# Kernel optimization log

Hardware: AMD Instinct MI355X
Metric: run time of the kernel (lower is better)

Reference implementation:

```python
import jax, jax.numpy as jnp
import numpy as np

C_SINGLE = 768
C_PAIR = 128
NUM_HEADS = 16
D_HEAD = C_SINGLE // NUM_HEADS
LC = 1024


def setup_inputs() -> dict:
    key = jax.random.key(0)
    ks = jax.random.split(key, 16)
    s = jax.random.normal(ks[0], (LC, C_SINGLE), dtype=jnp.float32)
    z = jax.random.normal(ks[1], (LC, LC, C_PAIR), dtype=jnp.float32)
    pd_mask = jax.random.randint(ks[2], (LC, LC), 0, 2) > 0
    pd_mask = pd_mask | jnp.eye(LC, dtype=bool)  # ensure every row has a valid key
    dist_bias_h = jax.random.normal(ks[3], (LC, LC, NUM_HEADS), dtype=jnp.float32)
    prior_bias = jax.random.normal(ks[4], (LC, LC), dtype=jnp.float32)
    def lin_w(k):
        return jax.random.normal(k, (C_SINGLE, C_SINGLE), dtype=jnp.float32) * 0.02
    def lin_b(k):
        return jax.random.normal(k, (C_SINGLE,), dtype=jnp.float32) * 0.02
    return {
        "s": s, "z": z, "pd_mask": pd_mask,
        "dist_bias_h": dist_bias_h, "prior_bias": prior_bias,
        "Wq": lin_w(ks[5]), "bq": lin_b(ks[6]),
        "Wk": lin_w(ks[7]), "bk": lin_b(ks[8]),
        "Wv": lin_w(ks[9]), "bv": lin_b(ks[10]),
        "Wz": jax.random.normal(ks[11], (C_PAIR, NUM_HEADS), dtype=jnp.float32) * 0.02,
        "Wo": lin_w(ks[12]), "bo": lin_b(ks[13]),
        "Wg": lin_w(ks[14]), "bg": lin_b(ks[15]),
    }


def reference(s, z, pd_mask, dist_bias_h, prior_bias,
              Wq, bq, Wk, bk, Wv, bv, Wz, Wo, bo, Wg, bg):
    Lc = s.shape[0]
    H, d = NUM_HEADS, D_HEAD
    # projections, split heads -> [H, Lc, d]
    qh = (s @ Wq + bq).reshape(Lc, H, d).transpose(1, 0, 2)
    kh = (s @ Wk + bk).reshape(Lc, H, d).transpose(1, 0, 2)
    vh = (s @ Wv + bv).reshape(Lc, H, d).transpose(1, 0, 2)
    scale = 1.0 / (d ** 0.5)
    # fp32 logits (module forces fp32 for attention block)
    logits = jnp.einsum('hid,hjd->hij',
                        qh.astype(jnp.float32), kh.astype(jnp.float32)) * scale
    # pair bias: [Lc,Lc,c_pair] @ [c_pair,H] -> [H,Lc,Lc]
    logits = logits + jnp.einsum('ijc,ch->hij', z.astype(jnp.float32), Wz)
    logits = logits + dist_bias_h.astype(jnp.float32).transpose(2, 0, 1)
    logits = logits + prior_bias.astype(jnp.float32)[None]
    neg_inf = jnp.finfo(jnp.float32).min
    logits = jnp.where(pd_mask[None], logits, neg_inf)
    attn = jax.nn.softmax(logits, axis=-1)
    # dropout is identity in eval mode
    attn_c = attn.astype(s.dtype)
    ctx = jnp.einsum('hij,hjd->hid', attn_c, vh)
    ctx = ctx.transpose(1, 0, 2).reshape(Lc, H * d)
    gate = jax.nn.sigmoid(s @ Wg + bg)
    y = gate * (ctx @ Wo + bo)
    return y, attn_c
```

## Files before the change

kernel.cpp:

```cpp
#include <hip/hip_runtime.h>
#include <hip/hip_bf16.h>
#include <float.h>

#define LC 1024
#define CS 768
#define NH 16
#define DH 48
#define CP 128

typedef __attribute__((ext_vector_type(8))) short short8;
typedef __attribute__((ext_vector_type(4))) float f32x4;
typedef __attribute__((ext_vector_type(4))) unsigned short ushort4v;

__device__ inline unsigned short f2b(float f){
    unsigned u = __builtin_bit_cast(unsigned, f);
    unsigned r = 0x7FFFu + ((u >> 16) & 1u);
    return (unsigned short)((u + r) >> 16);
}

__global__ void k_convert(const float* __restrict__ src, unsigned short* __restrict__ dst, int n){
    int i = (blockIdx.x * blockDim.x + threadIdx.x) * 4;
    if (i < n){
        float4 v = *reinterpret_cast<const float4*>(src + i);
        ushort4v o;
        o[0] = f2b(v.x); o[1] = f2b(v.y); o[2] = f2b(v.z); o[3] = f2b(v.w);
        *reinterpret_cast<ushort4v*>(dst + i) = o;
    }
}

struct P5 { const float* s[5]; unsigned short* d[5]; };

__global__ void k_transpose_w5(P5 p){
    __shared__ float t[32][33];
    int m = blockIdx.z;
    const float* W = p.s[m];
    unsigned short* O = p.d[m];
    int i0 = blockIdx.x * 32, o0 = blockIdx.y * 32;
    int tx = threadIdx.x & 31, ty = threadIdx.x >> 5;
    for (int r = 0; r < 32; r += 8)
        t[ty + r][tx] = W[(long)(i0 + ty + r) * CS + o0 + tx];
    __syncthreads();
    for (int r = 0; r < 32; r += 8)
        O[(long)(o0 + ty + r) * CS + i0 + tx] = f2b(t[tx][ty + r]);
}

__global__ void k_transpose_v(const unsigned short* __restrict__ v, unsigned short* __restrict__ vt){
    __shared__ unsigned short t[32][33];
    int j0 = blockIdx.x * 32, c0 = blockIdx.y * 32;
    int tx = threadIdx.x & 31, ty = threadIdx.x >> 5;
    for (int r = 0; r < 32; r += 8)
        t[ty + r][tx] = v[(long)(j0 + ty + r) * CS + c0 + tx];
    __syncthreads();
    for (int r = 0; r < 32; r += 8)
        vt[(long)(c0 + ty + r) * LC + j0 + tx] = t[tx][ty + r];
}

__global__ __launch_bounds__(256) void k_gemm(
    const unsigned short* __restrict__ A,
    const unsigned short* __restrict__ B,
    const float* __restrict__ bias,
    void* __restrict__ out,
    const float* __restrict__ gate,
    int mode)
{
    __shared__ unsigned short As[64][40];
    __shared__ unsigned short Bs[64][40];
    int m0 = blockIdx.x * 64, n0 = blockIdx.y * 64;
    int t = threadIdx.x, lane = t & 63, w = t >> 6;
    int l15 = lane & 15, l4 = lane >> 4;
    f32x4 zero4 = {0.f, 0.f, 0.f, 0.f};
    f32x4 acc[4] = {zero4, zero4, zero4, zero4};

    for (int kk = 0; kk < CS; kk += 32){
        int row = t >> 2, c = (t & 3) * 8;
        *reinterpret_cast<short8*>(&As[row][c]) =
            *reinterpret_cast<const short8*>(&A[(long)(m0 + row) * CS + kk + c]);
        *reinterpret_cast<short8*>(&Bs[row][c]) =
            *reinterpret_cast<const short8*>(&B[(long)(n0 + row) * CS + kk + c]);
        __syncthreads();
        short8 af = *reinterpret_cast<const short8*>(&As[w * 16 + l15][l4 * 8]);
        for (int nt = 0; nt < 4; nt++){
            short8 bf = *reinterpret_cast<const short8*>(&Bs[nt * 16 + l15][l4 * 8]);
            acc[nt] = __builtin_amdgcn_mfma_f32_16x16x32_bf16(af, bf, acc[nt], 0, 0, 0);
        }
        __syncthreads();
    }
    for (int nt = 0; nt < 4; nt++){
        int col = n0 + nt * 16 + l15;
        float bv = bias[col];
        for (int r = 0; r < 4; r++){
            int rowi = m0 + w * 16 + l4 * 4 + r;
            float v = acc[nt][r] + bv;
            if (mode <= 2){
                ((unsigned short*)out)[(long)rowi * CS + col] = f2b(v);
            } else if (mode == 3){
                ((float*)out)[(long)rowi * CS + col] = 1.0f / (1.0f + expf(-v));
            } else {
                ((float*)out)[(long)rowi * CS + col] = gate[(long)rowi * CS + col] * v;
            }
        }
    }
}

__global__ __launch_bounds__(512) void k_logits(
    const float* __restrict__ z,
    const float* __restrict__ Wz,
    const unsigned short* __restrict__ qb,
    const unsigned short* __restrict__ kb,
    const float* __restrict__ dist,
    const float* __restrict__ prior,
    const int* __restrict__ mask,
    float* __restrict__ attn,
    float* __restrict__ stats)
{
    __shared__ float Ls[16][16][17];
    __shared__ float dist_s[16][16][17];
    __shared__ float prior_s[16][16];
    __shared__ int   mask_s[16][16];

    int I0 = blockIdx.x * 16;
    int chunk = blockIdx.y;
    int t = threadIdx.x, lane = t & 63, w = t >> 6;
    int l15 = lane & 15, l4 = lane >> 4;
    const float scale = 0.14433756729740643f;

    short8 wzf[4];
    for (int ck = 0; ck < 4; ck++){
        short8 f;
        for (int b = 0; b < 8; b++){
            int c = ck * 32 + l4 * 8 + b;
            f[b] = (short)f2b(Wz[c * 16 + l15]);
        }
        wzf[ck] = f;
    }
    short8 qf0[2], qf1[2];
    for (int rep = 0; rep < 2; rep++){
        int h = w * 2 + rep;
        const unsigned short* qrow = qb + (long)(I0 + l15) * CS + h * 48;
        qf0[rep] = *reinterpret_cast<const short8*>(qrow + l4 * 8);
        short8 zz; for (int b = 0; b < 8; b++) zz[b] = 0;
        qf1[rep] = zz;
        if (l4 < 2) qf1[rep] = *reinterpret_cast<const short8*>(qrow + 32 + l4 * 8);
    }

    float mreg[8], sreg[8];
    for (int p = 0; p < 8; p++){ mreg[p] = -FLT_MAX; sreg[p] = 0.f; }

    for (int jt = 0; jt < 8; jt++){
        int j0 = chunk * 128 + jt * 16;

        for (int rep = 0; rep < 2; rep++){
            int i = w * 2 + rep;
            f32x4 acc = {0.f, 0.f, 0.f, 0.f};
            const float* zrow = z + ((long)(I0 + i) * LC + (j0 + l15)) * CP;
            for (int ck = 0; ck < 4; ck++){
                float4 z0 = *reinterpret_cast<const float4*>(zrow + ck * 32 + l4 * 8);
                float4 z1 = *reinterpret_cast<const float4*>(zrow + ck * 32 + l4 * 8 + 4);
                short8 zf;
                zf[0] = f2b(z0.x); zf[1] = f2b(z0.y); zf[2] = f2b(z0.z); zf[3] = f2b(z0.w);
                zf[4] = f2b(z1.x); zf[5] = f2b(z1.y); zf[6] = f2b(z1.z); zf[7] = f2b(z1.w);
                acc = __builtin_amdgcn_mfma_f32_16x16x32_bf16(zf, wzf[ck], acc, 0, 0, 0);
            }
            for (int r = 0; r < 4; r++) Ls[i][l4 * 4 + r][l15] = acc[r];
        }
        {
            int s = t * 8;
            int di = s >> 8, rem = s & 255;
            const float* src = dist + (((long)(I0 + di) * LC + j0) * NH) + rem;
            float4 d0 = *reinterpret_cast<const float4*>(src);
            float4 d1 = *reinterpret_cast<const float4*>(src + 4);
            float dv[8] = {d0.x, d0.y, d0.z, d0.w, d1.x, d1.y, d1.z, d1.w};
            for (int b = 0; b < 8; b++){
                int jj = (rem + b) >> 4, hh = (rem + b) & 15;
                dist_s[di][jj][hh] = dv[b];
            }
            if (t < 256){
                int ii = t >> 4, jj = t & 15;
                prior_s[ii][jj] = prior[(long)(I0 + ii) * LC + j0 + jj];
                mask_s[ii][jj]  = mask [(long)(I0 + ii) * LC + j0 + jj];
            }
        }
        __syncthreads();

        for (int rep = 0; rep < 2; rep++){
            int h = w * 2 + rep;
            const unsigned short* krow = kb + (long)(j0 + l15) * CS + h * 48;
            short8 kf0 = *reinterpret_cast<const short8*>(krow + l4 * 8);
            short8 kf1; for (int b = 0; b < 8; b++) kf1[b] = 0;
            if (l4 < 2) kf1 = *reinterpret_cast<const short8*>(krow + 32 + l4 * 8);
            f32x4 acc = {0.f, 0.f, 0.f, 0.f};
            acc = __builtin_amdgcn_mfma_f32_16x16x32_bf16(qf0[rep], kf0, acc, 0, 0, 0);
            acc = __builtin_amdgcn_mfma_f32_16x16x32_bf16(qf1[rep], kf1, acc, 0, 0, 0);
            for (int r = 0; r < 4; r++)
                Ls[l4 * 4 + r][l15][h] += acc[r] * scale;
        }
        __syncthreads();

        int qw = t >> 4, jl = t & 15;
        for (int p = 0; p < 8; p++){
            int task = p * 32 + qw;
            int ti = task >> 4, th = task & 15;
            float lg = Ls[ti][jl][th] + dist_s[ti][jl][th] + prior_s[ti][jl];
            bool mk = (mask_s[ti][jl] != 0);
            lg = mk ? lg : -FLT_MAX;
            attn[(long)th * LC * LC + (long)(I0 + ti) * LC + j0 + jl] = lg;
            float mt = lg;
            for (int mo = 1; mo < 16; mo <<= 1) mt = fmaxf(mt, __shfl_xor(mt, mo));
            float e = mk ? expf(lg - mt) : 0.f;
            float st = e;
            for (int mo = 1; mo < 16; mo <<= 1) st += __shfl_xor(st, mo);
            if (mt > mreg[p]){
                sreg[p] = sreg[p] * expf(mreg[p] - mt) + st;
                mreg[p] = mt;
            } else {
                sreg[p] += st * expf(mt - mreg[p]);
            }
        }
        __syncthreads();
    }
    if ((t & 15) == 0){
        int qw = t >> 4;
        for (int p = 0; p < 8; p++){
            int task = p * 32 + qw;
            int ti = task >> 4, th = task & 15;
            long off = (((long)th * LC + (I0 + ti)) * 8 + chunk) * 2;
            stats[off]     = mreg[p];
            stats[off + 1] = sreg[p];
        }
    }
}

__global__ __launch_bounds__(256) void k_ctx(
    float* __restrict__ attn,
    const unsigned short* __restrict__ vt,
    const float* __restrict__ stats,
    unsigned short* __restrict__ ctx)
{
    int h = blockIdx.x, ib = blockIdx.y;
    int t = threadIdx.x, lane = t & 63, w = t >> 6;
    int l15 = lane & 15, l4 = lane >> 4;
    int i = ib * 64 + w * 16 + l15;

    const float* sp = stats + ((long)h * LC + i) * 16;
    float M = -FLT_MAX;
    for (int c = 0; c < 8; c++) M = fmaxf(M, sp[c * 2]);
    float S = 0.f;
    for (int c = 0; c < 8; c++) S += sp[c * 2 + 1] * expf(sp[c * 2] - M);
    float invS = 1.0f / S;

    f32x4 zero4 = {0.f, 0.f, 0.f, 0.f};
    f32x4 acc[3] = {zero4, zero4, zero4};
    float* arow = attn + (long)h * LC * LC + (long)i * LC;

    for (int jk = 0; jk < LC; jk += 32){
        float4 a0 = *reinterpret_cast<const float4*>(arow + jk + l4 * 8);
        float4 a1 = *reinterpret_cast<const float4*>(arow + jk + l4 * 8 + 4);
        float p[8] = {a0.x, a0.y, a0.z, a0.w, a1.x, a1.y, a1.z, a1.w};
        short8 pf;
        for (int b = 0; b < 8; b++){
            float e = expf(p[b] - M) * invS;
            p[b] = e;
            pf[b] = (short)f2b(e);
        }
        float4 o0 = {p[0], p[1], p[2], p[3]}, o1 = {p[4], p[5], p[6], p[7]};
        *reinterpret_cast<float4*>(arow + jk + l4 * 8) = o0;
        *reinterpret_cast<float4*>(arow + jk + l4 * 8 + 4) = o1;
        for (int dt = 0; dt < 3; dt++){
            const unsigned short* vrow = vt + (long)(h * 48 + dt * 16 + l15) * LC + jk + l4 * 8;
            short8 bf = *reinterpret_cast<const short8*>(vrow);
            acc[dt] = __builtin_amdgcn_mfma_f32_16x16x32_bf16(pf, bf, acc[dt], 0, 0, 0);
        }
    }
    for (int dt = 0; dt < 3; dt++)
        for (int r = 0; r < 4; r++){
            int rowi = ib * 64 + w * 16 + l4 * 4 + r;
            ctx[(long)rowi * CS + h * 48 + dt * 16 + l15] = f2b(acc[dt][r]);
        }
}

extern "C" void kernel_launch(void* const* d_in, const int* in_sizes, int n_in,
                              void* d_out, int out_size, void* d_ws, size_t ws_size,
                              hipStream_t stream)
{
    const float* s     = (const float*)d_in[0];
    const float* z     = (const float*)d_in[1];
    const int*   mask  = (const int*)  d_in[2];
    const float* dist  = (const float*)d_in[3];
    const float* prior = (const float*)d_in[4];
    const float* Wq = (const float*)d_in[5];  const float* bq = (const float*)d_in[6];
    const float* Wk = (const float*)d_in[7];  const float* bk = (const float*)d_in[8];
    const float* Wv = (const float*)d_in[9];  const float* bv = (const float*)d_in[10];
    const float* Wz = (const float*)d_in[11];
    const float* Wo = (const float*)d_in[12]; const float* bo = (const float*)d_in[13];
    const float* Wg = (const float*)d_in[14]; const float* bg = (const float*)d_in[15];

    char* ws = (char*)d_ws;
    const size_t SZ_BF = (size_t)LC * CS * 2;
    const size_t SZ_WT = (size_t)CS * CS * 2;
    unsigned short* sb   = (unsigned short*)(ws);
    unsigned short* wqt  = (unsigned short*)(ws + SZ_BF);
    unsigned short* wkt  = (unsigned short*)(ws + SZ_BF + SZ_WT);
    unsigned short* wvt  = (unsigned short*)(ws + SZ_BF + 2 * SZ_WT);
    unsigned short* wgt  = (unsigned short*)(ws + SZ_BF + 3 * SZ_WT);
    unsigned short* wot  = (unsigned short*)(ws + SZ_BF + 4 * SZ_WT);
    unsigned short* qb   = (unsigned short*)(ws + SZ_BF + 5 * SZ_WT);
    unsigned short* kb   = (unsigned short*)(ws + 2 * SZ_BF + 5 * SZ_WT);
    unsigned short* vb   = (unsigned short*)(ws + 3 * SZ_BF + 5 * SZ_WT);
    unsigned short* vt   = (unsigned short*)(ws + 4 * SZ_BF + 5 * SZ_WT);
    float*          gate = (float*)        (ws + 5 * SZ_BF + 5 * SZ_WT);
    unsigned short* ctxb = (unsigned short*)(ws + 5 * SZ_BF + 5 * SZ_WT + (size_t)LC * CS * 4);
    float*          stats= (float*)        (ws + 6 * SZ_BF + 5 * SZ_WT + (size_t)LC * CS * 4);

    float* y    = (float*)d_out;
    float* attn = (float*)d_out + (size_t)LC * CS;

    k_convert<<<768, 256, 0, stream>>>(s, sb, LC * CS);
    P5 p;
    p.s[0] = Wq; p.s[1] = Wk; p.s[2] = Wv; p.s[3] = Wg; p.s[4] = Wo;
    p.d[0] = wqt; p.d[1] = wkt; p.d[2] = wvt; p.d[3] = wgt; p.d[4] = wot;
    k_transpose_w5<<<dim3(24, 24, 5), 256, 0, stream>>>(p);

    k_gemm<<<dim3(16, 12), 256, 0, stream>>>(sb, wqt, bq, qb, nullptr, 0);
    k_gemm<<<dim3(16, 12), 256, 0, stream>>>(sb, wkt, bk, kb, nullptr, 1);
    k_gemm<<<dim3(16, 12), 256, 0, stream>>>(sb, wvt, bv, vb, nullptr, 2);
    k_gemm<<<dim3(16, 12), 256, 0, stream>>>(sb, wgt, bg, gate, nullptr, 3);
    k_transpose_v<<<dim3(32, 24), 256, 0, stream>>>(vb, vt);

    k_logits<<<dim3(64, 8), 512, 0, stream>>>(z, Wz, qb, kb, dist, prior, mask, attn, stats);
    k_ctx<<<dim3(16, 16), 256, 0, stream>>>(attn, vt, stats, ctxb);
    k_gemm<<<dim3(16, 12), 256, 0, stream>>>(ctxb, wot, bo, y, gate, 4);
}
```

Measured before the change: 1.004 ms.

## Fuse QKVG GEMMs, prefetch z/dist in logits, split ctx over key halves

Merges the four projection GEMMs into one launch over concatenated transposed weights. In the logits kernel, it register-prefetches the next tile's z, dist, prior and mask, drops one barrier by writing QK scores to a separate shared buffer, and uses fast exp with a branchless online-softmax update. The ctx kernel splits the key range across two waves and reduces them through shared memory, doubling the grid for more parallelism. The trade-offs are higher register pressure and a launch_bounds occupancy hint in the logits kernel, plus slightly less precise exponentials.

```diff
diff --git a/kernel.cpp b/kernel.cpp
--- a/kernel.cpp
+++ b/kernel.cpp
@@ -55,13 +55,61 @@
         vt[(long)(c0 + ty + r) * LC + j0 + tx] = t[tx][ty + r];
 }
 
-__global__ __launch_bounds__(256) void k_gemm(
+__global__ __launch_bounds__(256) void k_gemm_qkvg(
+    const unsigned short* __restrict__ A,
+    const unsigned short* __restrict__ B,
+    const float* __restrict__ bq, const float* __restrict__ bk,
+    const float* __restrict__ bv, const float* __restrict__ bg,
+    unsigned short* __restrict__ oq, unsigned short* __restrict__ ok,
+    unsigned short* __restrict__ ov, float* __restrict__ og)
+{
+    __shared__ unsigned short As[64][40];
+    __shared__ unsigned short Bs[64][40];
+    int m0 = blockIdx.x * 64, n0 = blockIdx.y * 64;
+    int seg = blockIdx.y / 12;
+    int ncol0 = n0 - seg * CS;
+    int t = threadIdx.x, lane = t & 63, w = t >> 6;
+    int l15 = lane & 15, l4 = lane >> 4;
+    f32x4 zero4 = {0.f, 0.f, 0.f, 0.f};
+    f32x4 acc[4] = {zero4, zero4, zero4, zero4};
+
+    for (int kk = 0; kk < CS; kk += 32){
+        int row = t >> 2, c = (t & 3) * 8;
+        *reinterpret_cast<short8*>(&As[row][c]) =
+            *reinterpret_cast<const short8*>(&A[(long)(m0 + row) * CS + kk + c]);
+        *reinterpret_cast<short8*>(&Bs[row][c]) =
+            *reinterpret_cast<const short8*>(&B[(long)(n0 + row) * CS + kk + c]);
+        __syncthreads();
+        short8 af = *reinterpret_cast<const short8*>(&As[w * 16 + l15][l4 * 8]);
+        for (int nt = 0; nt < 4; nt++){
+            short8 bf = *reinterpret_cast<const short8*>(&Bs[nt * 16 + l15][l4 * 8]);
+            acc[nt] = __builtin_amdgcn_mfma_f32_16x16x32_bf16(af, bf, acc[nt], 0, 0, 0);
+        }
+        __syncthreads();
+    }
+    const float* bias = (seg == 0) ? bq : (seg == 1) ? bk : (seg == 2) ? bv : bg;
+    unsigned short* obf = (seg == 0) ? oq : (seg == 1) ? ok : ov;
+    for (int nt = 0; nt < 4; nt++){
+        int col = ncol0 + nt * 16 + l15;
+        float bvv = bias[col];
+        for (int r = 0; r < 4; r++){
+            int rowi = m0 + w * 16 + l4 * 4 + r;
+            float v = acc[nt][r] + bvv;
+            if (seg < 3){
+                obf[(long)rowi * CS + col] = f2b(v);
+            } else {
+                og[(long)rowi * CS + col] = 1.0f / (1.0f + __expf(-v));
+            }
+        }
+    }
+}
+
+__global__ __launch_bounds__(256) void k_gemm_out(
     const unsigned short* __restrict__ A,
     const unsigned short* __restrict__ B,
     const float* __restrict__ bias,
-    void* __restrict__ out,
     const float* __restrict__ gate,
-    int mode)
+    float* __restrict__ out)
 {
     __shared__ unsigned short As[64][40];
     __shared__ unsigned short Bs[64][40];
@@ -87,22 +135,15 @@
     }
     for (int nt = 0; nt < 4; nt++){
         int col = n0 + nt * 16 + l15;
-        float bv = bias[col];
+        float bvv = bias[col];
         for (int r = 0; r < 4; r++){
             int rowi = m0 + w * 16 + l4 * 4 + r;
-            float v = acc[nt][r] + bv;
-            if (mode <= 2){
-                ((unsigned short*)out)[(long)rowi * CS + col] = f2b(v);
-            } else if (mode == 3){
-                ((float*)out)[(long)rowi * CS + col] = 1.0f / (1.0f + expf(-v));
-            } else {
-                ((float*)out)[(long)rowi * CS + col] = gate[(long)rowi * CS + col] * v;
-            }
-        }
-    }
-}
-
-__global__ __launch_bounds__(512) void k_logits(
+            out[(long)rowi * CS + col] = gate[(long)rowi * CS + col] * (acc[nt][r] + bvv);
+        }
+    }
+}
+
+__global__ __launch_bounds__(512, 4) void k_logits(
     const float* __restrict__ z,
     const float* __restrict__ Wz,
     const unsigned short* __restrict__ qb,
@@ -113,7 +154,8 @@
     float* __restrict__ attn,
     float* __restrict__ stats)
 {
-    __shared__ float Ls[16][16][17];
+    __shared__ float Ls [16][16][17];
+    __shared__ float Ls2[16][16][17];
     __shared__ float dist_s[16][16][17];
     __shared__ float prior_s[16][16];
     __shared__ int   mask_s[16][16];
@@ -146,42 +188,86 @@
     float mreg[8], sreg[8];
     for (int p = 0; p < 8; p++){ mreg[p] = -FLT_MAX; sreg[p] = 0.f; }
 
+    float4 pf[8];
+    float4 dd0, dd1;
+    float pp = 0.f; int mm = 0;
+    int sofs = t * 8, di = sofs >> 8, rem = sofs & 255;
+    int pr_i = t >> 4, pr_j = t & 15;
+
+    int row0 = I0 + w * 2;
+
     for (int jt = 0; jt < 8; jt++){
         int j0 = chunk * 128 + jt * 16;
 
-        for (int rep = 0; rep < 2; rep++){
-            int i = w * 2 + rep;
+        if (jt == 0){
+            const float* zr = z + ((long)row0 * LC + (j0 + l15)) * CP + l4 * 8;
+            pf[0] = *(const float4*)(zr);      pf[1] = *(const float4*)(zr + 4);
+            pf[2] = *(const float4*)(zr + 32); pf[3] = *(const float4*)(zr + 36);
+            pf[4] = *(const float4*)(zr + 64); pf[5] = *(const float4*)(zr + 68);
+            pf[6] = *(const float4*)(zr + 96); pf[7] = *(const float4*)(zr + 100);
+            const float* dsrc = dist + (((long)(I0 + di) * LC + j0) * NH) + rem;
+            dd0 = *(const float4*)dsrc; dd1 = *(const float4*)(dsrc + 4);
+            if (t < 256){
+                pp = prior[(long)(I0 + pr_i) * LC + j0 + pr_j];
+                mm = mask [(long)(I0 + pr_i) * LC + j0 + pr_j];
+            }
+        }
+
+        {
+            float dv[8] = {dd0.x, dd0.y, dd0.z, dd0.w, dd1.x, dd1.y, dd1.z, dd1.w};
+            #pragma unroll
+            for (int b = 0; b < 8; b++){
+                int jj = (rem + b) >> 4, hh = (rem + b) & 15;
+                dist_s[di][jj][hh] = dv[b];
+            }
+            if (t < 256){ prior_s[pr_i][pr_j] = pp; mask_s[pr_i][pr_j] = mm; }
+        }
+
+        {
             f32x4 acc = {0.f, 0.f, 0.f, 0.f};
-            const float* zrow = z + ((long)(I0 + i) * LC + (j0 + l15)) * CP;
+            #pragma unroll
             for (int ck = 0; ck < 4; ck++){
-                float4 z0 = *reinterpret_cast<const float4*>(zrow + ck * 32 + l4 * 8);
-                float4 z1 = *reinterpret_cast<const float4*>(zrow + ck * 32 + l4 * 8 + 4);
+                float4 z0 = pf[ck * 2], z1 = pf[ck * 2 + 1];
                 short8 zf;
                 zf[0] = f2b(z0.x); zf[1] = f2b(z0.y); zf[2] = f2b(z0.z); zf[3] = f2b(z0.w);
                 zf[4] = f2b(z1.x); zf[5] = f2b(z1.y); zf[6] = f2b(z1.z); zf[7] = f2b(z1.w);
                 acc = __builtin_amdgcn_mfma_f32_16x16x32_bf16(zf, wzf[ck], acc, 0, 0, 0);
             }
-            for (int r = 0; r < 4; r++) Ls[i][l4 * 4 + r][l15] = acc[r];
+            #pragma unroll
+            for (int r = 0; r < 4; r++) Ls[w * 2][l4 * 4 + r][l15] = acc[r];
         }
         {
-            int s = t * 8;
-            int di = s >> 8, rem = s & 255;
-            const float* src = dist + (((long)(I0 + di) * LC + j0) * NH) + rem;
-            float4 d0 = *reinterpret_cast<const float4*>(src);
-            float4 d1 = *reinterpret_cast<const float4*>(src + 4);
-            float dv[8] = {d0.x, d0.y, d0.z, d0.w, d1.x, d1.y, d1.z, d1.w};
-            for (int b = 0; b < 8; b++){
-                int jj = (rem + b) >> 4, hh = (rem + b) & 15;
-                dist_s[di][jj][hh] = dv[b];
-            }
+            const float* zr = z + ((long)(row0 + 1) * LC + (j0 + l15)) * CP + l4 * 8;
+            f32x4 acc = {0.f, 0.f, 0.f, 0.f};
+            #pragma unroll
+            for (int ck = 0; ck < 4; ck++){
+                float4 z0 = *(const float4*)(zr + ck * 32);
+                float4 z1 = *(const float4*)(zr + ck * 32 + 4);
+                short8 zf;
+                zf[0] = f2b(z0.x); zf[1] = f2b(z0.y); zf[2] = f2b(z0.z); zf[3] = f2b(z0.w);
+                zf[4] = f2b(z1.x); zf[5] = f2b(z1.y); zf[6] = f2b(z1.z); zf[7] = f2b(z1.w);
+                acc = __builtin_amdgcn_mfma_f32_16x16x32_bf16(zf, wzf[ck], acc, 0, 0, 0);
+            }
+            #pragma unroll
+            for (int r = 0; r < 4; r++) Ls[w * 2 + 1][l4 * 4 + r][l15] = acc[r];
+        }
+
+        if (jt < 7){
+            int j0n = j0 + 16;
+            const float* zr = z + ((long)row0 * LC + (j0n + l15)) * CP + l4 * 8;
+            pf[0] = *(const float4*)(zr);      pf[1] = *(const float4*)(zr + 4);
+            pf[2] = *(const float4*)(zr + 32); pf[3] = *(const float4*)(zr + 36);
+            pf[4] = *(const float4*)(zr + 64); pf[5] = *(const float4*)(zr + 68);
+            pf[6] = *(const float4*)(zr + 96); pf[7] = *(const float4*)(zr + 100);
+            const float* dsrc = dist + (((long)(I0 + di) * LC + j0n) * NH) + rem;
+            dd0 = *(const float4*)dsrc; dd1 = *(const float4*)(dsrc + 4);
             if (t < 256){
-                int ii = t >> 4, jj = t & 15;
-                prior_s[ii][jj] = prior[(long)(I0 + ii) * LC + j0 + jj];
-                mask_s[ii][jj]  = mask [(long)(I0 + ii) * LC + j0 + jj];
-            }
-        }
-        __syncthreads();
-
+                pp = prior[(long)(I0 + pr_i) * LC + j0n + pr_j];
+                mm = mask [(long)(I0 + pr_i) * LC + j0n + pr_j];
+            }
+        }
+
+        #pragma unroll
         for (int rep = 0; rep < 2; rep++){
             int h = w * 2 + rep;
             const unsigned short* krow = kb + (long)(j0 + l15) * CS + h * 48;
@@ -191,35 +277,35 @@
             f32x4 acc = {0.f, 0.f, 0.f, 0.f};
             acc = __builtin_amdgcn_mfma_f32_16x16x32_bf16(qf0[rep], kf0, acc, 0, 0, 0);
             acc = __builtin_amdgcn_mfma_f32_16x16x32_bf16(qf1[rep], kf1, acc, 0, 0, 0);
+            #pragma unroll
             for (int r = 0; r < 4; r++)
-                Ls[l4 * 4 + r][l15][h] += acc[r] * scale;
+                Ls2[l4 * 4 + r][l15][h] = acc[r] * scale;
         }
         __syncthreads();
 
         int qw = t >> 4, jl = t & 15;
+        #pragma unroll
         for (int p = 0; p < 8; p++){
             int task = p * 32 + qw;
             int ti = task >> 4, th = task & 15;
-            float lg = Ls[ti][jl][th] + dist_s[ti][jl][th] + prior_s[ti][jl];
+            float lg = Ls[ti][jl][th] + Ls2[ti][jl][th] + dist_s[ti][jl][th] + prior_s[ti][jl];
             bool mk = (mask_s[ti][jl] != 0);
             lg = mk ? lg : -FLT_MAX;
             attn[(long)th * LC * LC + (long)(I0 + ti) * LC + j0 + jl] = lg;
             float mt = lg;
             for (int mo = 1; mo < 16; mo <<= 1) mt = fmaxf(mt, __shfl_xor(mt, mo));
-            float e = mk ? expf(lg - mt) : 0.f;
+            float e = mk ? __expf(lg - mt) : 0.f;
             float st = e;
             for (int mo = 1; mo < 16; mo <<= 1) st += __shfl_xor(st, mo);
-            if (mt > mreg[p]){
-                sreg[p] = sreg[p] * expf(mreg[p] - mt) + st;
-                mreg[p] = mt;
-            } else {
-                sreg[p] += st * expf(mt - mreg[p]);
-            }
+            float mnew = fmaxf(mreg[p], mt);
+            sreg[p] = sreg[p] * __expf(mreg[p] - mnew) + st * __expf(mt - mnew);
+            mreg[p] = mnew;
         }
         __syncthreads();
     }
     if ((t & 15) == 0){
         int qw = t >> 4;
+        #pragma unroll
         for (int p = 0; p < 8; p++){
             int task = p * 32 + qw;
             int ti = task >> 4, th = task & 15;
@@ -236,46 +322,63 @@
     const float* __restrict__ stats,
     unsigned short* __restrict__ ctx)
 {
+    __shared__ float red[2][16][49];
     int h = blockIdx.x, ib = blockIdx.y;
     int t = threadIdx.x, lane = t & 63, w = t >> 6;
     int l15 = lane & 15, l4 = lane >> 4;
-    int i = ib * 64 + w * 16 + l15;
+    int wg = w >> 1, jh = w & 1;
+    int i = ib * 32 + wg * 16 + l15;
 
     const float* sp = stats + ((long)h * LC + i) * 16;
     float M = -FLT_MAX;
     for (int c = 0; c < 8; c++) M = fmaxf(M, sp[c * 2]);
     float S = 0.f;
-    for (int c = 0; c < 8; c++) S += sp[c * 2 + 1] * expf(sp[c * 2] - M);
+    for (int c = 0; c < 8; c++) S += sp[c * 2 + 1] * __expf(sp[c * 2] - M);
     float invS = 1.0f / S;
 
     f32x4 zero4 = {0.f, 0.f, 0.f, 0.f};
     f32x4 acc[3] = {zero4, zero4, zero4};
     float* arow = attn + (long)h * LC * LC + (long)i * LC;
 
-    for (int jk = 0; jk < LC; jk += 32){
+    for (int jk = jh * 512; jk < jh * 512 + 512; jk += 32){
         float4 a0 = *reinterpret_cast<const float4*>(arow + jk + l4 * 8);
         float4 a1 = *reinterpret_cast<const float4*>(arow + jk + l4 * 8 + 4);
         float p[8] = {a0.x, a0.y, a0.z, a0.w, a1.x, a1.y, a1.z, a1.w};
-        short8 pf;
+        short8 pfr;
+        #pragma unroll
         for (int b = 0; b < 8; b++){
-            float e = expf(p[b] - M) * invS;
+            float e = __expf(p[b] - M) * invS;
             p[b] = e;
-            pf[b] = (short)f2b(e);
+            pfr[b] = (short)f2b(e);
         }
         float4 o0 = {p[0], p[1], p[2], p[3]}, o1 = {p[4], p[5], p[6], p[7]};
         *reinterpret_cast<float4*>(arow + jk + l4 * 8) = o0;
         *reinterpret_cast<float4*>(arow + jk + l4 * 8 + 4) = o1;
+        #pragma unroll
         for (int dt = 0; dt < 3; dt++){
             const unsigned short* vrow = vt + (long)(h * 48 + dt * 16 + l15) * LC + jk + l4 * 8;
             short8 bf = *reinterpret_cast<const short8*>(vrow);
-            acc[dt] = __builtin_amdgcn_mfma_f32_16x16x32_bf16(pf, bf, acc[dt], 0, 0, 0);
-        }
-    }
-    for (int dt = 0; dt < 3; dt++)
-        for (int r = 0; r < 4; r++){
-            int rowi = ib * 64 + w * 16 + l4 * 4 + r;
-            ctx[(long)rowi * CS + h * 48 + dt * 16 + l15] = f2b(acc[dt][r]);
-        }
+            acc[dt] = __builtin_amdgcn_mfma_f32_16x16x32_bf16(pfr, bf, acc[dt], 0, 0, 0);
+        }
+    }
+    if (jh == 1){
+        #pragma unroll
+        for (int dt = 0; dt < 3; dt++)
+            #pragma unroll
+            for (int r = 0; r < 4; r++)
+                red[wg][l4 * 4 + r][dt * 16 + l15] = acc[dt][r];
+    }
+    __syncthreads();
+    if (jh == 0){
+        #pragma unroll
+        for (int dt = 0; dt < 3; dt++)
+            #pragma unroll
+            for (int r = 0; r < 4; r++){
+                float v = acc[dt][r] + red[wg][l4 * 4 + r][dt * 16 + l15];
+                int rowi = ib * 32 + wg * 16 + l4 * 4 + r;
+                ctx[(long)rowi * CS + h * 48 + dt * 16 + l15] = f2b(v);
+            }
+    }
 }
 
 extern "C" void kernel_launch(void* const* d_in, const int* in_sizes, int n_in,
@@ -298,10 +401,7 @@
     const size_t SZ_BF = (size_t)LC * CS * 2;
     const size_t SZ_WT = (size_t)CS * CS * 2;
     unsigned short* sb   = (unsigned short*)(ws);
-    unsigned short* wqt  = (unsigned short*)(ws + SZ_BF);
-    unsigned short* wkt  = (unsigned short*)(ws + SZ_BF + SZ_WT);
-    unsigned short* wvt  = (unsigned short*)(ws + SZ_BF + 2 * SZ_WT);
-    unsigned short* wgt  = (unsigned short*)(ws + SZ_BF + 3 * SZ_WT);
+    unsigned short* wcat = (unsigned short*)(ws + SZ_BF);
     unsigned short* wot  = (unsigned short*)(ws + SZ_BF + 4 * SZ_WT);
     unsigned short* qb   = (unsigned short*)(ws + SZ_BF + 5 * SZ_WT);
     unsigned short* kb   = (unsigned short*)(ws + 2 * SZ_BF + 5 * SZ_WT);
@@ -317,16 +417,17 @@
     k_convert<<<768, 256, 0, stream>>>(s, sb, LC * CS);
     P5 p;
     p.s[0] = Wq; p.s[1] = Wk; p.s[2] = Wv; p.s[3] = Wg; p.s[4] = Wo;
-    p.d[0] = wqt; p.d[1] = wkt; p.d[2] = wvt; p.d[3] = wgt; p.d[4] = wot;
+    p.d[0] = wcat;
+    p.d[1] = wcat + (size_t)CS * CS;
+    p.d[2] = wcat + 2 * (size_t)CS * CS;
+    p.d[3] = wcat + 3 * (size_t)CS * CS;
+    p.d[4] = wot;
     k_transpose_w5<<<dim3(24, 24, 5), 256, 0, stream>>>(p);
 
-    k_gemm<<<dim3(16, 12), 256, 0, stream>>>(sb, wqt, bq, qb, nullptr, 0);
-    k_gemm<<<dim3(16, 12), 256, 0, stream>>>(sb, wkt, bk, kb, nullptr, 1);
-    k_gemm<<<dim3(16, 12), 256, 0, stream>>>(sb, wvt, bv, vb, nullptr, 2);
-    k_gemm<<<dim3(16, 12), 256, 0, stream>>>(sb, wgt, bg, gate, nullptr, 3);
+    k_gemm_qkvg<<<dim3(16, 48), 256, 0, stream>>>(sb, wcat, bq, bk, bv, bg, qb, kb, vb, gate);
     k_transpose_v<<<dim3(32, 24), 256, 0, stream>>>(vb, vt);
 
     k_logits<<<dim3(64, 8), 512, 0, stream>>>(z, Wz, qb, kb, dist, prior, mask, attn, stats);
-    k_ctx<<<dim3(16, 16), 256, 0, stream>>>(attn, vt, stats, ctxb);
-    k_gemm<<<dim3(16, 12), 256, 0, stream>>>(ctxb, wot, bo, y, gate, 4);
-}
+    k_ctx<<<dim3(16, 32), 256, 0, stream>>>(attn, vt, stats, ctxb);
+    k_gemm_out<<<dim3(16, 12), 256, 0, stream>>>(ctxb, wot, bo, gate, y);
+}
```

Result: faster. 967.1 us (-3.7%).
